# Performance work log

Hardware: AMD Instinct MI355X
Metric: run time of the kernel (lower is better)

## Reference

```python
import jax, jax.numpy as jnp
import numpy as np

TIMESTEPS = 32
MAX_LATENCY = 1.0


def setup_inputs() -> dict:
    key = jax.random.key(0)
    data = jax.random.uniform(key, (32, 256, 256), dtype=jnp.float32)
    return {"data": data}


def reference(data):
    # data: [B, H, W] (any trailing dims). Output: [B, T, H, W].
    T = TIMESTEPS
    d_min = data.min()
    d_max = data.max()
    denom = jnp.maximum(d_max - d_min, jnp.asarray(1e-12, data.dtype))
    normalized = jnp.where(d_max > d_min, (data - d_min) / denom,
                           jnp.full_like(data, 0.5))
    latencies = (1.0 - normalized) * MAX_LATENCY
    # torch .long() truncates toward zero; latencies >= 0 so floor == trunc
    spike_times = jnp.clip((latencies * (T - 1)).astype(jnp.int32), 0, T - 1)
    # one-hot over timestep axis, then move it next to batch: [B, ..., T] -> [B, T, ...]
    spike_train = jax.nn.one_hot(spike_times, T, dtype=jnp.float32)
    return jnp.moveaxis(spike_train, -1, 1)
```

## Files before the change

### kernel.cpp

```cpp
#include <hip/hip_runtime.h>

#define TSTEPS 32
#define HW 65536
#define NB 32
#define N_ELEM (NB * HW)
#define N4 (N_ELEM / 4)

__device__ __forceinline__ unsigned int f2key(float f) {
    unsigned int u = __float_as_uint(f);
    return (u & 0x80000000u) ? ~u : (u | 0x80000000u);
}
__device__ __forceinline__ float key2f(unsigned int k) {
    unsigned int u = (k & 0x80000000u) ? (k & 0x7fffffffu) : ~k;
    return __uint_as_float(u);
}

__global__ void lc_init_ws(unsigned int* ws) {
    if (threadIdx.x == 0) {
        ws[0] = 0xFFFFFFFFu;
        ws[1] = 0x00000000u;
    }
}

__global__ void lc_minmax(const float4* __restrict__ in, unsigned int* __restrict__ ws) {
    __shared__ unsigned int smin[4], smax[4];
    unsigned int kmin = 0xFFFFFFFFu, kmax = 0u;
    int stride = gridDim.x * blockDim.x;
    for (int i = blockIdx.x * blockDim.x + threadIdx.x; i < N4; i += stride) {
        float4 v = in[i];
        unsigned int k;
        k = f2key(v.x); kmin = min(kmin, k); kmax = max(kmax, k);
        k = f2key(v.y); kmin = min(kmin, k); kmax = max(kmax, k);
        k = f2key(v.z); kmin = min(kmin, k); kmax = max(kmax, k);
        k = f2key(v.w); kmin = min(kmin, k); kmax = max(kmax, k);
    }
    #pragma unroll
    for (int off = 32; off >= 1; off >>= 1) {
        kmin = min(kmin, (unsigned int)__shfl_xor((int)kmin, off, 64));
        kmax = max(kmax, (unsigned int)__shfl_xor((int)kmax, off, 64));
    }
    int wave = threadIdx.x >> 6;
    if ((threadIdx.x & 63) == 0) { smin[wave] = kmin; smax[wave] = kmax; }
    __syncthreads();
    if (threadIdx.x == 0) {
        #pragma unroll
        for (int w = 1; w < 4; ++w) {
            kmin = min(kmin, smin[w]);
            kmax = max(kmax, smax[w]);
        }
        atomicMin(&ws[0], kmin);
        atomicMax(&ws[1], kmax);
    }
}

__device__ __forceinline__ int spike_t(float x, float mn, float denom, bool valid) {
    float n   = valid ? ((x - mn) / denom) : 0.5f;
    float lat = 1.0f - n;
    int   t   = (int)(lat * 31.0f);
    t = t < 0 ? 0 : t;
    t = t > (TSTEPS - 1) ? (TSTEPS - 1) : t;
    return t;
}

__global__ void lc_spike(const float4* __restrict__ in, float* __restrict__ out,
                         const unsigned int* __restrict__ ws) {
    float mn = key2f(ws[0]);
    float mx = key2f(ws[1]);
    bool  valid = (mx > mn);
    float denom = fmaxf(mx - mn, 1e-12f);

    int idx = blockIdx.x * blockDim.x + threadIdx.x;
    if (idx >= N4) return;
    int b   = idx >> 14;
    int rem = idx & 16383;

    float4 v = in[idx];
    int t0 = spike_t(v.x, mn, denom, valid);
    int t1 = spike_t(v.y, mn, denom, valid);
    int t2 = spike_t(v.z, mn, denom, valid);
    int t3 = spike_t(v.w, mn, denom, valid);

    float* base = out + (size_t)b * TSTEPS * HW + (size_t)rem * 4;
    #pragma unroll
    for (int tt = 0; tt < TSTEPS; ++tt) {
        float4 o;
        o.x = (tt == t0) ? 1.0f : 0.0f;
        o.y = (tt == t1) ? 1.0f : 0.0f;
        o.z = (tt == t2) ? 1.0f : 0.0f;
        o.w = (tt == t3) ? 1.0f : 0.0f;
        *reinterpret_cast<float4*>(base + (size_t)tt * HW) = o;
    }
}

extern "C" void kernel_launch(void* const* d_in, const int* in_sizes, int n_in,
                              void* d_out, int out_size, void* d_ws, size_t ws_size,
                              hipStream_t stream) {
    const float4*  in = (const float4*)d_in[0];
    float*        out = (float*)d_out;
    unsigned int*  ws = (unsigned int*)d_ws;

    lc_init_ws<<<1, 64, 0, stream>>>(ws);
    lc_minmax<<<256, 256, 0, stream>>>(in, ws);
    lc_spike<<<(N4 + 255) / 256, 256, 0, stream>>>(in, out, ws);
}
```

Before: 57.19 us.

## Use nontemporal output stores, memset-based workspace init, and wider minmax grid

The init kernel is replaced by a hipMemsetAsync that sets both workspace words to all-ones. Max is tracked as the min of the inverted key, so both reductions can use atomicMin from that one init value. The minmax grid grows from 256 to 1024 blocks to spread the 8MB read across more CUs. The 256MB one-hot output is written with nontemporal stores so streaming writes bypass cache retention; a memset may still cost about as much as a tiny kernel launch.

```diff
diff --git a/kernel.cpp b/kernel.cpp
--- a/kernel.cpp
+++ b/kernel.cpp
@@ -5,6 +5,8 @@
 #define NB 32
 #define N_ELEM (NB * HW)
 #define N4 (N_ELEM / 4)
+
+typedef float vf4 __attribute__((ext_vector_type(4)));
 
 __device__ __forceinline__ unsigned int f2key(float f) {
     unsigned int u = __float_as_uint(f);
@@ -15,41 +17,34 @@
     return __uint_as_float(u);
 }
 
-__global__ void lc_init_ws(unsigned int* ws) {
-    if (threadIdx.x == 0) {
-        ws[0] = 0xFFFFFFFFu;
-        ws[1] = 0x00000000u;
-    }
-}
-
 __global__ void lc_minmax(const float4* __restrict__ in, unsigned int* __restrict__ ws) {
-    __shared__ unsigned int smin[4], smax[4];
-    unsigned int kmin = 0xFFFFFFFFu, kmax = 0u;
+    __shared__ unsigned int smin[4], sinvmax[4];
+    unsigned int kmin = 0xFFFFFFFFu, kinv = 0xFFFFFFFFu;
     int stride = gridDim.x * blockDim.x;
     for (int i = blockIdx.x * blockDim.x + threadIdx.x; i < N4; i += stride) {
         float4 v = in[i];
         unsigned int k;
-        k = f2key(v.x); kmin = min(kmin, k); kmax = max(kmax, k);
-        k = f2key(v.y); kmin = min(kmin, k); kmax = max(kmax, k);
-        k = f2key(v.z); kmin = min(kmin, k); kmax = max(kmax, k);
-        k = f2key(v.w); kmin = min(kmin, k); kmax = max(kmax, k);
+        k = f2key(v.x); kmin = min(kmin, k); kinv = min(kinv, ~k);
+        k = f2key(v.y); kmin = min(kmin, k); kinv = min(kinv, ~k);
+        k = f2key(v.z); kmin = min(kmin, k); kinv = min(kinv, ~k);
+        k = f2key(v.w); kmin = min(kmin, k); kinv = min(kinv, ~k);
     }
     #pragma unroll
     for (int off = 32; off >= 1; off >>= 1) {
         kmin = min(kmin, (unsigned int)__shfl_xor((int)kmin, off, 64));
-        kmax = max(kmax, (unsigned int)__shfl_xor((int)kmax, off, 64));
+        kinv = min(kinv, (unsigned int)__shfl_xor((int)kinv, off, 64));
     }
     int wave = threadIdx.x >> 6;
-    if ((threadIdx.x & 63) == 0) { smin[wave] = kmin; smax[wave] = kmax; }
+    if ((threadIdx.x & 63) == 0) { smin[wave] = kmin; sinvmax[wave] = kinv; }
     __syncthreads();
     if (threadIdx.x == 0) {
         #pragma unroll
         for (int w = 1; w < 4; ++w) {
             kmin = min(kmin, smin[w]);
-            kmax = max(kmax, smax[w]);
+            kinv = min(kinv, sinvmax[w]);
         }
         atomicMin(&ws[0], kmin);
-        atomicMax(&ws[1], kmax);
+        atomicMin(&ws[1], kinv);
     }
 }
 
@@ -65,7 +60,7 @@
 __global__ void lc_spike(const float4* __restrict__ in, float* __restrict__ out,
                          const unsigned int* __restrict__ ws) {
     float mn = key2f(ws[0]);
-    float mx = key2f(ws[1]);
+    float mx = key2f(~ws[1]);
     bool  valid = (mx > mn);
     float denom = fmaxf(mx - mn, 1e-12f);
 
@@ -83,12 +78,12 @@
     float* base = out + (size_t)b * TSTEPS * HW + (size_t)rem * 4;
     #pragma unroll
     for (int tt = 0; tt < TSTEPS; ++tt) {
-        float4 o;
+        vf4 o;
         o.x = (tt == t0) ? 1.0f : 0.0f;
         o.y = (tt == t1) ? 1.0f : 0.0f;
         o.z = (tt == t2) ? 1.0f : 0.0f;
         o.w = (tt == t3) ? 1.0f : 0.0f;
-        *reinterpret_cast<float4*>(base + (size_t)tt * HW) = o;
+        __builtin_nontemporal_store(o, reinterpret_cast<vf4*>(base + (size_t)tt * HW));
     }
 }
 
@@ -99,7 +94,7 @@
     float*        out = (float*)d_out;
     unsigned int*  ws = (unsigned int*)d_ws;
 
-    lc_init_ws<<<1, 64, 0, stream>>>(ws);
-    lc_minmax<<<256, 256, 0, stream>>>(in, ws);
+    (void)hipMemsetAsync(ws, 0xFF, 2 * sizeof(unsigned int), stream);
+    lc_minmax<<<1024, 256, 0, stream>>>(in, ws);
     lc_spike<<<(N4 + 255) / 256, 256, 0, stream>>>(in, out, ws);
 }
```

Result: slower. 83.66 us (+46.3%).
